# Performance work log

Hardware: AMD Instinct MI355X
Metric: run time of the kernel (lower is better)

The kernel has to match this reference:

```python
import jax, jax.numpy as jnp
import numpy as np

B, V, L, C, H = 2, 8, 256, 1024, 16

def setup_inputs() -> dict:
    key = jax.random.key(0)
    ks = jax.random.split(key, 6)
    s = 0.02  # init scale for weights
    x = jax.random.normal(ks[0], (B, V, L, C), jnp.float32)
    Wq = jax.random.normal(ks[1], (C, C), jnp.float32) * s
    Wk = jax.random.normal(ks[2], (C, C), jnp.float32) * s
    Wv = jax.random.normal(ks[3], (C, C), jnp.float32) * s
    Wp = jax.random.normal(ks[4], (C, C), jnp.float32) * s
    bp = jnp.zeros((C,), jnp.float32)
    return {"x": x, "Wq": Wq, "Wk": Wk, "Wv": Wv, "Wp": Wp, "bp": bp}

def _view_mask(V, L):
    # view-level allow mask, expanded to token level [S, S]
    vi = jnp.arange(V)
    qv, kv = vi[:, None], vi[None, :]
    cross = ((qv == 0) & (kv == 1)) | ((qv == 1) & (kv == 0))
    later = (qv > 1) | (kv > 1)
    allow = cross | (later & (qv >= kv))  # [V, V]
    return jnp.repeat(jnp.repeat(allow, L, axis=0), L, axis=1)  # [V*L, V*L]

def reference(x, Wq, Wk, Wv, Wp, bp):
    b, v, l, c = x.shape
    h = H
    dh = c // h
    scale = dh ** -0.5
    s = v * l
    xf = x.reshape(b, s, c)
    # torch Linear: y = x @ W.T
    q = (xf @ Wq.T).reshape(b, s, h, dh).transpose(0, 2, 1, 3)  # [b,h,s,dh]
    k = (xf @ Wk.T).reshape(b, s, h, dh).transpose(0, 2, 1, 3)
    vv = (xf @ Wv.T).reshape(b, s, h, dh).transpose(0, 2, 1, 3)
    scores = jnp.einsum('bhqd,bhkd->bhqk', q, k) * scale  # [b,h,s,s]
    mask = _view_mask(v, l)
    scores = jnp.where(mask, scores, -jnp.inf)
    attn = jax.nn.softmax(scores, axis=-1)
    out = jnp.einsum('bhqk,bhkd->bhqd', attn, vv)
    out = out.transpose(0, 2, 1, 3).reshape(b, v, l, c)
    return out @ Wp.T + bp
```

## Files before the change

### kernel.cpp

```cpp
#include <hip/hip_runtime.h>
#include <stdint.h>

typedef unsigned short ushort_t;
typedef __attribute__((ext_vector_type(8))) __bf16 bf16x8;
typedef __attribute__((ext_vector_type(4))) float floatx4;

__device__ __forceinline__ ushort_t f2bf(float f) {
    uint32_t u = __builtin_bit_cast(uint32_t, f);
    u += 0x7fffu + ((u >> 16) & 1u);
    return (ushort_t)(u >> 16);
}

typedef __attribute__((address_space(1))) const void glb_void;
typedef __attribute__((address_space(3))) void lds_void;
__device__ __forceinline__ void gld16(const void* g, void* l) {
    __builtin_amdgcn_global_load_lds((glb_void*)g, (lds_void*)l, 16, 0, 0);
}

#define QSCALE 0.18033688011112042f

__global__ void cast_kernel(const float* __restrict__ x,
                            const float* __restrict__ Wq, const float* __restrict__ Wk,
                            const float* __restrict__ Wv, const float* __restrict__ Wp,
                            ushort_t* __restrict__ xb, ushort_t* __restrict__ Wqkvb,
                            ushort_t* __restrict__ Wpb)
{
    const int64_t NX = 4194304, NW = 1048576;
    int64_t i4 = ((int64_t)blockIdx.x * blockDim.x + threadIdx.x) * 4;
    const float* src; ushort_t* dst; int64_t off;
    if (i4 < NX)            { src = x;  dst = xb;          off = i4; }
    else if (i4 < NX+NW)    { src = Wq; dst = Wqkvb;       off = i4 - NX; }
    else if (i4 < NX+2*NW)  { src = Wk; dst = Wqkvb + NW;  off = i4 - NX - NW; }
    else if (i4 < NX+3*NW)  { src = Wv; dst = Wqkvb + 2*NW;off = i4 - NX - 2*NW; }
    else                    { src = Wp; dst = Wpb;         off = i4 - NX - 3*NW; }
    float4 v = *(const float4*)(src + off);
    ushort4 o;
    o.x = f2bf(v.x); o.y = f2bf(v.y); o.z = f2bf(v.z); o.w = f2bf(v.w);
    *(ushort4*)(dst + off) = o;
}

#define BM 128
#define BN 128
#define BK 32

__global__ __launch_bounds__(256, 3)
void gemm_bt(const ushort_t* __restrict__ A, const ushort_t* __restrict__ Bmat,
             int M, int N, int K, int mode,
             ushort_t* __restrict__ qb, ushort_t* __restrict__ kb, ushort_t* __restrict__ vtb,
             float* __restrict__ outf, const float* __restrict__ bias)
{
    __shared__ ushort_t As[BM * BK];
    __shared__ ushort_t Bs[BN * BK];
    const int tid  = threadIdx.x;
    const int lane = tid & 63;
    const int wave = tid >> 6;
    const int m0 = blockIdx.x * BM;
    const int n0 = blockIdx.y * BN;
    const int wrow = (wave >> 1) * 64;
    const int wcol = (wave & 1) * 64;
    const int q_ = lane >> 4;
    const int ml = lane & 15;

    floatx4 acc[4][4];
    for (int i = 0; i < 4; i++) for (int j = 0; j < 4; j++) acc[i][j] = floatx4{0.f,0.f,0.f,0.f};

    const int t0 = wave * 2, t1 = wave * 2 + 1;
    const int row_l = lane >> 2;
    const int col_l = (lane & 3) * 8;
    const ushort_t* Ag0 = A    + (int64_t)(m0 + t0*16 + row_l) * K + col_l;
    const ushort_t* Ag1 = A    + (int64_t)(m0 + t1*16 + row_l) * K + col_l;
    const ushort_t* Bg0 = Bmat + (int64_t)(n0 + t0*16 + row_l) * K + col_l;
    const ushort_t* Bg1 = Bmat + (int64_t)(n0 + t1*16 + row_l) * K + col_l;
    ushort_t* Al0 = As + t0*512; ushort_t* Al1 = As + t1*512;
    ushort_t* Bl0 = Bs + t0*512; ushort_t* Bl1 = Bs + t1*512;

    for (int k0 = 0; k0 < K; k0 += BK) {
        __syncthreads();
        gld16(Ag0 + k0, Al0);
        gld16(Ag1 + k0, Al1);
        gld16(Bg0 + k0, Bl0);
        gld16(Bg1 + k0, Bl1);
        __syncthreads();
        bf16x8 af[4], bf[4];
        for (int mt = 0; mt < 4; mt++)
            af[mt] = *(const bf16x8*)(As + (wrow + mt*16 + ml) * BK + q_*8);
        for (int nt = 0; nt < 4; nt++)
            bf[nt] = *(const bf16x8*)(Bs + (wcol + nt*16 + ml) * BK + q_*8);
        for (int mt = 0; mt < 4; mt++)
            for (int nt = 0; nt < 4; nt++)
                acc[mt][nt] = __builtin_amdgcn_mfma_f32_16x16x32_bf16(af[mt], bf[nt], acc[mt][nt], 0, 0, 0);
    }

    if (mode == 0) {
        for (int mt = 0; mt < 4; mt++) for (int nt = 0; nt < 4; nt++) {
            floatx4 v = acc[mt][nt];
            int col = n0 + wcol + nt*16 + ml;
            int which = col >> 10;
            int nn = col & 1023;
            int h = nn >> 6, d = nn & 63;
            if (which < 2) {
                ushort_t* dst = (which == 0) ? qb : kb;
                float sc = (which == 0) ? QSCALE : 1.0f;
                for (int r = 0; r < 4; r++) {
                    int rowg = m0 + wrow + mt*16 + q_*4 + r;
                    int b = rowg >> 11, s = rowg & 2047;
                    dst[(((int64_t)(b*16 + h) * 2048 + s) << 6) + d] = f2bf(v[r] * sc);
                }
            } else {
                int rowg0 = m0 + wrow + mt*16 + q_*4;
                int b = rowg0 >> 11, sbase = rowg0 & 2047;
                ushort4 o;
                o.x = f2bf(v[0]); o.y = f2bf(v[1]); o.z = f2bf(v[2]); o.w = f2bf(v[3]);
                *(ushort4*)(vtb + (((int64_t)(b*16 + h) * 64 + d) << 11) + sbase) = o;
            }
        }
    } else {
        for (int mt = 0; mt < 4; mt++) for (int nt = 0; nt < 4; nt++) {
            floatx4 v = acc[mt][nt];
            int col = n0 + wcol + nt*16 + ml;
            float bv = bias[col];
            for (int r = 0; r < 4; r++) {
                int rowg = m0 + wrow + mt*16 + q_*4 + r;
                outf[(int64_t)rowg * N + col] = v[r] + bv;
            }
        }
    }
}

__global__ __launch_bounds__(256, 3)
void attn_kernel(const ushort_t* __restrict__ Q, const ushort_t* __restrict__ Kb,
                 const ushort_t* __restrict__ Vt, ushort_t* __restrict__ Out)
{
    __shared__ ushort_t Kl[8192];
    __shared__ ushort_t Vl[8192];
    __shared__ ushort_t Pl[4 * 16 * 136];

    int bi = blockIdx.x;
    int xcd = bi & 7;
    int sl  = bi >> 3;
    int bh  = xcd + 8 * (sl & 3);
    int rest = sl >> 2;
    int qv = 7 - (rest >> 2);
    int qt = rest & 3;
    int b = bh >> 4, h = bh & 15;
    int tid = threadIdx.x;
    int wave = tid >> 6, lane = tid & 63;
    int q_ = lane >> 4, ml = lane & 15;
    int rlane = lane & 15, clane = lane >> 4;
    int s0 = qv*256 + qt*64 + wave*16;

    const ushort_t* Kbh = Kb + ((int64_t)bh << 17);
    const ushort_t* Vbh = Vt + ((int64_t)bh << 17);
    ushort_t* Pw = Pl + wave * (16 * 136);

    const ushort_t* Qp = Q + (((int64_t)bh*2048 + s0 + ml) << 6) + q_*8;
    bf16x8 aq0 = *(const bf16x8*)(Qp);
    bf16x8 aq1 = *(const bf16x8*)(Qp + 32);

    floatx4 o_acc[4];
    for (int i = 0; i < 4; i++) o_acc[i] = floatx4{0.f,0.f,0.f,0.f};
    float lsum[4] = {0.f, 0.f, 0.f, 0.f};

    int views[8]; int nviews;
    if      (qv == 0) { views[0] = 1; nviews = 1; }
    else if (qv == 1) { views[0] = 0; nviews = 1; }
    else { nviews = qv + 1; for (int i = 0; i < nviews; i++) views[i] = i; }

    for (int vi = 0; vi < nviews; vi++) {
        int kb0 = views[vi] * 256;
        for (int ck = 0; ck < 2; ck++) {
            int koff = kb0 + ck * 128;

            __syncthreads();
            for (int i = 0; i < 4; i++) {
                int id = wave*4 + i;
                const ushort_t* gk = Kbh + (((int64_t)(koff + (id >> 1)*16 + rlane)) << 6)
                                         + (id & 1)*32 + clane*8;
                gld16(gk, Kl + id*512);
                const ushort_t* gv = Vbh + ((int64_t)((id & 3)*16 + rlane) << 11)
                                         + koff + (id >> 2)*32 + clane*8;
                gld16(gv, Vl + id*512);
            }
            __syncthreads();

            floatx4 sc[8];
            for (int kt = 0; kt < 8; kt++) {
                bf16x8 k0 = *(const bf16x8*)(Kl + kt*1024 + lane*8);
                bf16x8 k1 = *(const bf16x8*)(Kl + kt*1024 + 512 + lane*8);
                floatx4 cz = floatx4{0.f,0.f,0.f,0.f};
                cz = __builtin_amdgcn_mfma_f32_16x16x32_bf16(aq0, k0, cz, 0, 0, 0);
                cz = __builtin_amdgcn_mfma_f32_16x16x32_bf16(aq1, k1, cz, 0, 0, 0);
                sc[kt] = cz;
            }

            for (int kt = 0; kt < 8; kt++)
                for (int r = 0; r < 4; r++) {
                    float p = __builtin_amdgcn_exp2f(sc[kt][r]);
                    lsum[r] += p;
                    Pw[(q_*4 + r)*136 + kt*16 + ml] = f2bf(p);
                }

            asm volatile("s_waitcnt lgkmcnt(0)" ::: "memory");

            for (int g = 0; g < 4; g++) {
                bf16x8 ap = *(const bf16x8*)(Pw + ml*136 + g*32 + q_*8);
                for (int dt = 0; dt < 4; dt++) {
                    bf16x8 vv = *(const bf16x8*)(Vl + (g*4 + dt)*512 + lane*8);
                    o_acc[dt] = __builtin_amdgcn_mfma_f32_16x16x32_bf16(ap, vv, o_acc[dt], 0, 0, 0);
                }
            }
        }
    }

    for (int off = 1; off < 16; off <<= 1)
        for (int r = 0; r < 4; r++)
            lsum[r] += __shfl_xor(lsum[r], off);

    for (int dt = 0; dt < 4; dt++)
        for (int r = 0; r < 4; r++) {
            float v = o_acc[dt][r] / lsum[r];
            int sr = s0 + q_*4 + r;
            Out[((int64_t)b*2048 + sr) * 1024 + h*64 + dt*16 + ml] = f2bf(v);
        }
}

extern "C" void kernel_launch(void* const* d_in, const int* in_sizes, int n_in,
                              void* d_out, int out_size, void* d_ws, size_t ws_size,
                              hipStream_t stream) {
    const float* x  = (const float*)d_in[0];
    const float* Wq = (const float*)d_in[1];
    const float* Wk = (const float*)d_in[2];
    const float* Wv = (const float*)d_in[3];
    const float* Wp = (const float*)d_in[4];
    const float* bp = (const float*)d_in[5];
    float* out = (float*)d_out;

    char* ws = (char*)d_ws;
    ushort_t* xb    = (ushort_t*)(ws);
    ushort_t* Wqkvb = (ushort_t*)(ws + ((size_t)8  << 20));
    ushort_t* Wpb   = (ushort_t*)(ws + ((size_t)14 << 20));
    ushort_t* qb    = (ushort_t*)(ws + ((size_t)16 << 20));
    ushort_t* kbuf  = (ushort_t*)(ws + ((size_t)24 << 20));
    ushort_t* vtb   = (ushort_t*)(ws + ((size_t)40 << 20));
    ushort_t* attno = xb;

    cast_kernel<<<8192, 256, 0, stream>>>(x, Wq, Wk, Wv, Wp, xb, Wqkvb, Wpb);

    dim3 g0(4096 / BM, 3072 / BN);
    gemm_bt<<<g0, 256, 0, stream>>>(xb, Wqkvb, 4096, 3072, 1024, 0,
                                    qb, kbuf, vtb, nullptr, nullptr);

    attn_kernel<<<1024, 256, 0, stream>>>(qb, kbuf, vtb, attno);

    dim3 g1(4096 / BM, 1024 / BN);
    gemm_bt<<<g1, 256, 0, stream>>>(attno, Wpb, 4096, 1024, 1024, 1,
                                    nullptr, nullptr, nullptr, out, bp);
}
```

Before: 184.4 us.

## Process two query tiles per wave in attention and narrow output-projection GEMM tile

```diff
diff --git a/kernel.cpp b/kernel.cpp
--- a/kernel.cpp
+++ b/kernel.cpp
@@ -40,59 +40,64 @@
 }
 
 #define BM 128
-#define BN 128
 #define BK 32
 
+template<int BN_, int MODE>
 __global__ __launch_bounds__(256, 3)
 void gemm_bt(const ushort_t* __restrict__ A, const ushort_t* __restrict__ Bmat,
-             int M, int N, int K, int mode,
+             int M, int N, int K,
              ushort_t* __restrict__ qb, ushort_t* __restrict__ kb, ushort_t* __restrict__ vtb,
              float* __restrict__ outf, const float* __restrict__ bias)
 {
+    constexpr int NB_B = BN_ * BK / 512;
+    constexpr int NT   = BN_ / 32;
+    constexpr int PER_W = (8 + NB_B) / 4;
     __shared__ ushort_t As[BM * BK];
-    __shared__ ushort_t Bs[BN * BK];
+    __shared__ ushort_t Bs[BN_ * BK];
     const int tid  = threadIdx.x;
     const int lane = tid & 63;
     const int wave = tid >> 6;
     const int m0 = blockIdx.x * BM;
-    const int n0 = blockIdx.y * BN;
+    const int n0 = blockIdx.y * BN_;
     const int wrow = (wave >> 1) * 64;
-    const int wcol = (wave & 1) * 64;
+    const int wcol = (wave & 1) * (BN_ / 2);
     const int q_ = lane >> 4;
     const int ml = lane & 15;
 
-    floatx4 acc[4][4];
-    for (int i = 0; i < 4; i++) for (int j = 0; j < 4; j++) acc[i][j] = floatx4{0.f,0.f,0.f,0.f};
-
-    const int t0 = wave * 2, t1 = wave * 2 + 1;
+    floatx4 acc[4][NT];
+    for (int i = 0; i < 4; i++) for (int j = 0; j < NT; j++) acc[i][j] = floatx4{0.f,0.f,0.f,0.f};
+
     const int row_l = lane >> 2;
     const int col_l = (lane & 3) * 8;
-    const ushort_t* Ag0 = A    + (int64_t)(m0 + t0*16 + row_l) * K + col_l;
-    const ushort_t* Ag1 = A    + (int64_t)(m0 + t1*16 + row_l) * K + col_l;
-    const ushort_t* Bg0 = Bmat + (int64_t)(n0 + t0*16 + row_l) * K + col_l;
-    const ushort_t* Bg1 = Bmat + (int64_t)(n0 + t1*16 + row_l) * K + col_l;
-    ushort_t* Al0 = As + t0*512; ushort_t* Al1 = As + t1*512;
-    ushort_t* Bl0 = Bs + t0*512; ushort_t* Bl1 = Bs + t1*512;
+    const ushort_t* gptr[PER_W]; ushort_t* lptr[PER_W];
+    for (int i = 0; i < PER_W; i++) {
+        int id = wave * PER_W + i;
+        if (id < 8) {
+            gptr[i] = A + (int64_t)(m0 + id*16 + row_l) * K + col_l;
+            lptr[i] = As + id * 512;
+        } else {
+            int j = id - 8;
+            gptr[i] = Bmat + (int64_t)(n0 + j*16 + row_l) * K + col_l;
+            lptr[i] = Bs + j * 512;
+        }
+    }
 
     for (int k0 = 0; k0 < K; k0 += BK) {
         __syncthreads();
-        gld16(Ag0 + k0, Al0);
-        gld16(Ag1 + k0, Al1);
-        gld16(Bg0 + k0, Bl0);
-        gld16(Bg1 + k0, Bl1);
+        for (int i = 0; i < PER_W; i++) gld16(gptr[i] + k0, lptr[i]);
         __syncthreads();
-        bf16x8 af[4], bf[4];
+        bf16x8 af[4], bf[NT];
         for (int mt = 0; mt < 4; mt++)
             af[mt] = *(const bf16x8*)(As + (wrow + mt*16 + ml) * BK + q_*8);
-        for (int nt = 0; nt < 4; nt++)
+        for (int nt = 0; nt < NT; nt++)
             bf[nt] = *(const bf16x8*)(Bs + (wcol + nt*16 + ml) * BK + q_*8);
         for (int mt = 0; mt < 4; mt++)
-            for (int nt = 0; nt < 4; nt++)
+            for (int nt = 0; nt < NT; nt++)
                 acc[mt][nt] = __builtin_amdgcn_mfma_f32_16x16x32_bf16(af[mt], bf[nt], acc[mt][nt], 0, 0, 0);
     }
 
-    if (mode == 0) {
-        for (int mt = 0; mt < 4; mt++) for (int nt = 0; nt < 4; nt++) {
+    if constexpr (MODE == 0) {
+        for (int mt = 0; mt < 4; mt++) for (int nt = 0; nt < NT; nt++) {
             floatx4 v = acc[mt][nt];
             int col = n0 + wcol + nt*16 + ml;
             int which = col >> 10;
@@ -115,7 +120,7 @@
             }
         }
     } else {
-        for (int mt = 0; mt < 4; mt++) for (int nt = 0; nt < 4; nt++) {
+        for (int mt = 0; mt < 4; mt++) for (int nt = 0; nt < NT; nt++) {
             floatx4 v = acc[mt][nt];
             int col = n0 + wcol + nt*16 + ml;
             float bv = bias[col];
@@ -127,39 +132,43 @@
     }
 }
 
-__global__ __launch_bounds__(256, 3)
+__global__ __launch_bounds__(256, 2)
 void attn_kernel(const ushort_t* __restrict__ Q, const ushort_t* __restrict__ Kb,
                  const ushort_t* __restrict__ Vt, ushort_t* __restrict__ Out)
 {
     __shared__ ushort_t Kl[8192];
     __shared__ ushort_t Vl[8192];
-    __shared__ ushort_t Pl[4 * 16 * 136];
+    __shared__ ushort_t Pl[4 * 4096];
 
     int bi = blockIdx.x;
     int xcd = bi & 7;
     int sl  = bi >> 3;
     int bh  = xcd + 8 * (sl & 3);
     int rest = sl >> 2;
-    int qv = 7 - (rest >> 2);
-    int qt = rest & 3;
+    int qv = 7 - (rest >> 1);
+    int qt = rest & 1;
     int b = bh >> 4, h = bh & 15;
     int tid = threadIdx.x;
     int wave = tid >> 6, lane = tid & 63;
     int q_ = lane >> 4, ml = lane & 15;
     int rlane = lane & 15, clane = lane >> 4;
-    int s0 = qv*256 + qt*64 + wave*16;
+    int s0 = qv*256 + qt*128 + wave*32;
 
     const ushort_t* Kbh = Kb + ((int64_t)bh << 17);
     const ushort_t* Vbh = Vt + ((int64_t)bh << 17);
-    ushort_t* Pw = Pl + wave * (16 * 136);
-
-    const ushort_t* Qp = Q + (((int64_t)bh*2048 + s0 + ml) << 6) + q_*8;
-    bf16x8 aq0 = *(const bf16x8*)(Qp);
-    bf16x8 aq1 = *(const bf16x8*)(Qp + 32);
-
-    floatx4 o_acc[4];
-    for (int i = 0; i < 4; i++) o_acc[i] = floatx4{0.f,0.f,0.f,0.f};
-    float lsum[4] = {0.f, 0.f, 0.f, 0.f};
+    ushort_t* Pw = Pl + wave * 4096;
+
+    bf16x8 aq0[2], aq1[2];
+    for (int qf = 0; qf < 2; qf++) {
+        const ushort_t* Qp = Q + (((int64_t)bh*2048 + s0 + qf*16 + ml) << 6) + q_*8;
+        aq0[qf] = *(const bf16x8*)(Qp);
+        aq1[qf] = *(const bf16x8*)(Qp + 32);
+    }
+
+    floatx4 o_acc[2][4];
+    for (int qf = 0; qf < 2; qf++) for (int i = 0; i < 4; i++) o_acc[qf][i] = floatx4{0.f,0.f,0.f,0.f};
+    float lsum[2][4];
+    for (int qf = 0; qf < 2; qf++) for (int r = 0; r < 4; r++) lsum[qf][r] = 0.f;
 
     int views[8]; int nviews;
     if      (qv == 0) { views[0] = 1; nviews = 1; }
@@ -172,56 +181,69 @@
             int koff = kb0 + ck * 128;
 
             __syncthreads();
-            for (int i = 0; i < 4; i++) {
-                int id = wave*4 + i;
-                const ushort_t* gk = Kbh + (((int64_t)(koff + (id >> 1)*16 + rlane)) << 6)
-                                         + (id & 1)*32 + clane*8;
-                gld16(gk, Kl + id*512);
-                const ushort_t* gv = Vbh + ((int64_t)((id & 3)*16 + rlane) << 11)
-                                         + koff + (id >> 2)*32 + clane*8;
-                gld16(gv, Vl + id*512);
+            for (int i = 0; i < 8; i++) {
+                int id = wave*8 + i;
+                if (id < 16) {
+                    const ushort_t* gk = Kbh + (((int64_t)(koff + (id >> 1)*16 + rlane)) << 6)
+                                             + (id & 1)*32 + clane*8;
+                    gld16(gk, Kl + id*512);
+                } else {
+                    int id2 = id - 16;
+                    const ushort_t* gv = Vbh + ((int64_t)((id2 & 3)*16 + rlane) << 11)
+                                             + koff + (id2 >> 2)*32 + clane*8;
+                    gld16(gv, Vl + id2*512);
+                }
             }
             __syncthreads();
 
-            floatx4 sc[8];
+            floatx4 sc[2][8];
             for (int kt = 0; kt < 8; kt++) {
                 bf16x8 k0 = *(const bf16x8*)(Kl + kt*1024 + lane*8);
                 bf16x8 k1 = *(const bf16x8*)(Kl + kt*1024 + 512 + lane*8);
-                floatx4 cz = floatx4{0.f,0.f,0.f,0.f};
-                cz = __builtin_amdgcn_mfma_f32_16x16x32_bf16(aq0, k0, cz, 0, 0, 0);
-                cz = __builtin_amdgcn_mfma_f32_16x16x32_bf16(aq1, k1, cz, 0, 0, 0);
-                sc[kt] = cz;
-            }
-
-            for (int kt = 0; kt < 8; kt++)
-                for (int r = 0; r < 4; r++) {
-                    float p = __builtin_amdgcn_exp2f(sc[kt][r]);
-                    lsum[r] += p;
-                    Pw[(q_*4 + r)*136 + kt*16 + ml] = f2bf(p);
-                }
+                for (int qf = 0; qf < 2; qf++) {
+                    floatx4 cz = floatx4{0.f,0.f,0.f,0.f};
+                    cz = __builtin_amdgcn_mfma_f32_16x16x32_bf16(aq0[qf], k0, cz, 0, 0, 0);
+                    cz = __builtin_amdgcn_mfma_f32_16x16x32_bf16(aq1[qf], k1, cz, 0, 0, 0);
+                    sc[qf][kt] = cz;
+                }
+            }
+
+            for (int qf = 0; qf < 2; qf++)
+                for (int kt = 0; kt < 8; kt++)
+                    for (int r = 0; r < 4; r++) {
+                        float p = __builtin_amdgcn_exp2f(sc[qf][kt][r]);
+                        lsum[qf][r] += p;
+                        Pw[qf*2048 + kt*256 + (q_*4 + r)*16 + ml] = f2bf(p);
+                    }
 
             asm volatile("s_waitcnt lgkmcnt(0)" ::: "memory");
 
             for (int g = 0; g < 4; g++) {
-                bf16x8 ap = *(const bf16x8*)(Pw + ml*136 + g*32 + q_*8);
+                bf16x8 ap[2];
+                for (int qf = 0; qf < 2; qf++)
+                    ap[qf] = *(const bf16x8*)(Pw + qf*2048 + (2*g + (q_ >> 1))*256
+                                              + ml*16 + (q_ & 1)*8);
                 for (int dt = 0; dt < 4; dt++) {
                     bf16x8 vv = *(const bf16x8*)(Vl + (g*4 + dt)*512 + lane*8);
-                    o_acc[dt] = __builtin_amdgcn_mfma_f32_16x16x32_bf16(ap, vv, o_acc[dt], 0, 0, 0);
+                    for (int qf = 0; qf < 2; qf++)
+                        o_acc[qf][dt] = __builtin_amdgcn_mfma_f32_16x16x32_bf16(ap[qf], vv, o_acc[qf][dt], 0, 0, 0);
                 }
             }
         }
     }
 
     for (int off = 1; off < 16; off <<= 1)
-        for (int r = 0; r < 4; r++)
-            lsum[r] += __shfl_xor(lsum[r], off);
-
-    for (int dt = 0; dt < 4; dt++)
-        for (int r = 0; r < 4; r++) {
-            float v = o_acc[dt][r] / lsum[r];
-            int sr = s0 + q_*4 + r;
-            Out[((int64_t)b*2048 + sr) * 1024 + h*64 + dt*16 + ml] = f2bf(v);
-        }
+        for (int qf = 0; qf < 2; qf++)
+            for (int r = 0; r < 4; r++)
+                lsum[qf][r] += __shfl_xor(lsum[qf][r], off);
+
+    for (int qf = 0; qf < 2; qf++)
+        for (int dt = 0; dt < 4; dt++)
+            for (int r = 0; r < 4; r++) {
+                float v = o_acc[qf][dt][r] / lsum[qf][r];
+                int sr = s0 + qf*16 + q_*4 + r;
+                Out[((int64_t)b*2048 + sr) * 1024 + h*64 + dt*16 + ml] = f2bf(v);
+            }
 }
 
 extern "C" void kernel_launch(void* const* d_in, const int* in_sizes, int n_in,
@@ -246,13 +268,13 @@
 
     cast_kernel<<<8192, 256, 0, stream>>>(x, Wq, Wk, Wv, Wp, xb, Wqkvb, Wpb);
 
-    dim3 g0(4096 / BM, 3072 / BN);
-    gemm_bt<<<g0, 256, 0, stream>>>(xb, Wqkvb, 4096, 3072, 1024, 0,
-                                    qb, kbuf, vtb, nullptr, nullptr);
-
-    attn_kernel<<<1024, 256, 0, stream>>>(qb, kbuf, vtb, attno);
-
-    dim3 g1(4096 / BM, 1024 / BN);
-    gemm_bt<<<g1, 256, 0, stream>>>(attno, Wpb, 4096, 1024, 1024, 1,
-                                    nullptr, nullptr, nullptr, out, bp);
-}
+    dim3 g0(4096 / BM, 3072 / 128);
+    gemm_bt<128, 0><<<g0, 256, 0, stream>>>(xb, Wqkvb, 4096, 3072, 1024,
+                                            qb, kbuf, vtb, nullptr, nullptr);
+
+    attn_kernel<<<512, 256, 0, stream>>>(qb, kbuf, vtb, attno);
+
+    dim3 g1(4096 / BM, 1024 / 64);
+    gemm_bt<64, 1><<<g1, 256, 0, stream>>>(attno, Wpb, 4096, 1024, 1024,
+                                           nullptr, nullptr, nullptr, out, bp);
+}
```

Result: no change. 186.8 us (+1.3%).
